# Performance work log

Measured on AMD Instinct MI355X. Metric: run time of the kernel, lower is better.

Reference implementation:

```python
import jax, jax.numpy as jnp
import numpy as np

N = 1_000_000
INC = 128
OUTC = 128
NUM_SEG = 4096
GROUPS = 32
ACN_EPS = 1e-3      # ACN eps
CLAMP_MIN = 1e-3    # .clamp(min=0.001)
GN_EPS = 1e-5       # torch GroupNorm default eps


def setup_inputs() -> dict:
    key = jax.random.key(0)
    ks = jax.random.split(key, 8)
    x = jax.random.normal(ks[0], (N, INC), dtype=jnp.float32)
    weight_pri = jax.random.uniform(ks[1], (N,), dtype=jnp.float32)
    segment_idx = jnp.sort(jax.random.randint(ks[2], (N,), 0, NUM_SEG)).astype(jnp.int64)
    W_conv = (jax.random.normal(ks[3], (INC, OUTC), dtype=jnp.float32) * 0.02)
    b_conv = jnp.zeros((OUTC,), jnp.float32)
    W_att = (jax.random.normal(ks[4], (OUTC, 1), dtype=jnp.float32) * 0.02)
    b_att = jnp.zeros((1,), jnp.float32)
    gamma = jnp.ones((OUTC,), jnp.float32)
    beta = jnp.zeros((OUTC,), jnp.float32)
    return {"x": x, "weight_pri": weight_pri, "W_conv": W_conv, "b_conv": b_conv,
            "W_att": W_att, "b_att": b_att, "gamma": gamma, "beta": beta,
            "segment_idx": segment_idx}


def reference(x, weight_pri, W_conv, b_conv, W_att, b_att, gamma, beta, segment_idx):
    # conv: Linear(inc, outc)
    h = x @ W_conv + b_conv                                  # [N, OUTC]

    # --- ACN ---
    att = h @ W_att + b_att                                  # [N, 1]
    # scatter_softmax over segments (numerically stable)
    seg_max = jax.ops.segment_max(att, segment_idx, num_segments=NUM_SEG)
    e = jnp.exp(att - seg_max[segment_idx])
    a = e / jax.ops.segment_sum(e, segment_idx, num_segments=NUM_SEG)[segment_idx]
    a = a * weight_pri[:, None]
    denom = jnp.maximum(jax.ops.segment_sum(a, segment_idx, num_segments=NUM_SEG), CLAMP_MIN)
    a = a / denom[segment_idx]
    # segment-weighted mean / variance normalization
    mean = jax.ops.segment_sum(h * a, segment_idx, num_segments=NUM_SEG)   # [S, OUTC]
    out = h - mean[segment_idx]
    std = jnp.sqrt(jax.ops.segment_sum(a * out * out, segment_idx, num_segments=NUM_SEG) + ACN_EPS)
    out = out / std[segment_idx]

    # --- GroupNorm(32, OUTC) on [N, C]: normalize per sample, per group ---
    g = out.reshape(-1, GROUPS, OUTC // GROUPS)
    mu = g.mean(axis=-1, keepdims=True)
    var = g.var(axis=-1, keepdims=True)
    gn = ((g - mu) * jax.lax.rsqrt(var + GN_EPS)).reshape(-1, OUTC)
    gn = gn * gamma + beta

    return jax.nn.relu(gn), a
```

## Files before the change

### kernel.cpp

```cpp
#include <hip/hip_runtime.h>
#include <hip/hip_bf16.h>

#define NPTS 1000000
#define NSEG 4096
#define ATTCAP 2048

#define KS_ROWS 16
#define LPAD 136

typedef __attribute__((ext_vector_type(8))) short bf16x8;
typedef __attribute__((ext_vector_type(4))) float f32x4;
typedef __attribute__((ext_vector_type(2))) float f32x2;

__device__ __forceinline__ short f2bfs(float f) {
  union { __hip_bfloat16 b; unsigned short s; } u;
  u.b = __float2bfloat16(f);
  return (short)u.s;
}
__device__ __forceinline__ float bf2f(short h) {
  return __uint_as_float(((unsigned)(unsigned short)h) << 16);
}
__device__ __forceinline__ void online_merge(float& m, float& se, float& sw,
                                             float m2, float se2, float sw2) {
  float nm = fmaxf(m, m2);
  float f1 = __expf(m - nm), f2 = __expf(m2 - nm);
  se = se * f1 + se2 * f2;
  sw = sw * f1 + sw2 * f2;
  m = nm;
}

__device__ __forceinline__ int chbase_of(int wave, int lc) {
  return wave * 32 + (lc >> 1) * 4 + (lc & 1) * 2;
}

__device__ __forceinline__ void load_w2(const float* __restrict__ Wc, int chb, int lg,
                                        bf16x8 Bh[2][4], bf16x8 Bl[2][4]) {
#pragma unroll
  for (int ks = 0; ks < 4; ++ks) {
#pragma unroll
    for (int j = 0; j < 8; ++j) {
      int k = ks * 32 + lg * 8 + j;
      float2 w2 = *(const float2*)(Wc + (size_t)k * 128 + chb);
      float e[2] = {w2.x, w2.y};
#pragma unroll
      for (int c = 0; c < 2; ++c) {
        short hi = f2bfs(e[c]);
        Bh[c][ks][j] = hi;
        Bl[c][ks][j] = f2bfs(e[c] - bf2f(hi));
      }
    }
  }
}

__device__ __forceinline__ void cvt4(float4 v, short4& hi, short4& lo) {
  hi.x = f2bfs(v.x); lo.x = f2bfs(v.x - bf2f(hi.x));
  hi.y = f2bfs(v.y); lo.y = f2bfs(v.y - bf2f(hi.y));
  hi.z = f2bfs(v.z); lo.z = f2bfs(v.z - bf2f(hi.z));
  hi.w = f2bfs(v.w); lo.w = f2bfs(v.w - bf2f(hi.w));
}

__device__ __forceinline__ void cvt4v(f32x4 v, short4& hi, short4& lo) {
  hi.x = f2bfs(v[0]); lo.x = f2bfs(v[0] - bf2f(hi.x));
  hi.y = f2bfs(v[1]); lo.y = f2bfs(v[1] - bf2f(hi.y));
  hi.z = f2bfs(v[2]); lo.z = f2bfs(v[2] - bf2f(hi.z));
  hi.w = f2bfs(v[3]); lo.w = f2bfs(v[3] - bf2f(hi.w));
}

__device__ __forceinline__ void mfma_lds(const bf16x8* __restrict__ AHv,
                                         const bf16x8* __restrict__ ALv,
                                         int lc, int lg,
                                         const bf16x8 Bh[2][4], const bf16x8 Bl[2][4],
                                         f32x4 Cf[2]) {
  Cf[0] = (f32x4){0.f, 0.f, 0.f, 0.f};
  Cf[1] = (f32x4){0.f, 0.f, 0.f, 0.f};
#pragma unroll
  for (int ks = 0; ks < 4; ++ks) {
    int fi = lc * 17 + ks * 4 + lg;
    bf16x8 ah = AHv[fi];
    bf16x8 al = ALv[fi];
#pragma unroll
    for (int c = 0; c < 2; ++c) {
      Cf[c] = __builtin_amdgcn_mfma_f32_16x16x32_bf16(ah, Bh[c][ks], Cf[c], 0, 0, 0);
      Cf[c] = __builtin_amdgcn_mfma_f32_16x16x32_bf16(ah, Bl[c][ks], Cf[c], 0, 0, 0);
      Cf[c] = __builtin_amdgcn_mfma_f32_16x16x32_bf16(al, Bh[c][ks], Cf[c], 0, 0, 0);
    }
  }
}

__global__ __launch_bounds__(256, 4) void k_all2(
    const float* __restrict__ x, const float* __restrict__ wp,
    const float* __restrict__ Wc, const float* __restrict__ bc,
    const float* __restrict__ Wa,
    const float* __restrict__ gamma, const float* __restrict__ beta,
    const void* __restrict__ seg, float* __restrict__ out) {

  __shared__ float att_l[ATTCAP];
  __shared__ __align__(16) short AH[2][KS_ROWS * LPAD];
  __shared__ __align__(16) short AL[2][KS_ROWS * LPAD];
  __shared__ float us[128];
  __shared__ float sm_red[12];
  __shared__ int sm_flag;

  const int t = threadIdx.x;
  const int lane = t & 63;
  const int wave = t >> 6;
  const int lc = lane & 15;
  const int lg = lane >> 4;
  const int chb = chbase_of(wave, lc);
  const int s = blockIdx.x;
  const int* seg32 = (const int*)seg;

  if (t == 0) sm_flag = 0;
  __syncthreads();
  {
    int any = 0;
#pragma unroll
    for (int k = 0; k < 8; ++k) any |= seg32[2 * (t * 8 + k) + 1];
    if (any) sm_flag = 1;
  }
  __syncthreads();
  const int f64 = (sm_flag == 0);
  __syncthreads();

  int blo = 0, bhi = NPTS;
  while (blo < bhi) {
    int mid = (blo + bhi) >> 1;
    int v = f64 ? (int)((const long long*)seg)[mid] : seg32[mid];
    if (v < s) blo = mid + 1; else bhi = mid;
  }
  const int start = blo;
  bhi = NPTS;
  while (blo < bhi) {
    int mid = (blo + bhi) >> 1;
    int v = f64 ? (int)((const long long*)seg)[mid] : seg32[mid];
    if (v < s + 1) blo = mid + 1; else bhi = mid;
  }
  const int endc = min(blo, start + ATTCAP);
  if (start >= endc) return;
  const int len = endc - start;

  if (t < 128) {
    const float4* wa4 = (const float4*)Wa;
    const float4* wr  = (const float4*)(Wc + t * 128);
    float sv = 0.f;
#pragma unroll 8
    for (int c4 = 0; c4 < 32; ++c4) {
      float4 a = wr[c4], b = wa4[c4];
      sv += a.x * b.x + a.y * b.y + a.z * b.z + a.w * b.w;
    }
    us[t] = sv;
  }
  __syncthreads();

  {
    const int q8 = t & 7;
    float ur[16];
#pragma unroll
    for (int j = 0; j < 16; ++j) ur[j] = us[q8 * 16 + j];
    for (int r0 = start; r0 < endc; r0 += 32) {
      int row = r0 + (t >> 3);
      int ra = row < NPTS ? row : NPTS - 1;
      const float4* xp = (const float4*)(x + (size_t)ra * 128 + q8 * 16);
      float4 a0 = xp[0], b0 = xp[1], c0 = xp[2], d0 = xp[3];
      float sv = a0.x*ur[0] + a0.y*ur[1] + a0.z*ur[2] + a0.w*ur[3]
               + b0.x*ur[4] + b0.y*ur[5] + b0.z*ur[6] + b0.w*ur[7]
               + c0.x*ur[8] + c0.y*ur[9] + c0.z*ur[10]+ c0.w*ur[11]
               + d0.x*ur[12]+ d0.y*ur[13]+ d0.z*ur[14]+ d0.w*ur[15];
      sv += __shfl_xor(sv, 1, 64);
      sv += __shfl_xor(sv, 2, 64);
      sv += __shfl_xor(sv, 4, 64);
      if (q8 == 0 && row < endc) att_l[row - start] = sv;
    }
  }
  __syncthreads();

  float m = -3.0e38f, se = 0.f, sw = 0.f;
  for (int i = t; i < len; i += 256) {
    float av = att_l[i], w = wp[start + i];
    float nm = fmaxf(m, av);
    float sc = __expf(m - nm), e = __expf(av - nm);
    se = se * sc + e;
    sw = sw * sc + e * w;
    m = nm;
  }
#pragma unroll
  for (int o = 1; o < 64; o <<= 1)
    online_merge(m, se, sw, __shfl_xor(m, o, 64), __shfl_xor(se, o, 64), __shfl_xor(sw, o, 64));
  if (lane == 0) { sm_red[wave] = m; sm_red[4 + wave] = se; sm_red[8 + wave] = sw; }
  __syncthreads();
  float gmx = sm_red[0], gse = sm_red[4], gsw = sm_red[8];
#pragma unroll
  for (int i = 1; i < 4; ++i) online_merge(gmx, gse, gsw, sm_red[i], sm_red[4 + i], sm_red[8 + i]);
  const float ratio = gsw / gse;
  const float dn = fmaxf(ratio, 1e-3f);
  const float ka = 1.f / (gse * dn);
  const float Sa = ratio / dn;
  for (int i = t; i < len; i += 256) {
    float a = __expf(att_l[i] - gmx) * wp[start + i] * ka;
    att_l[i] = a;
    __builtin_nontemporal_store(a, out + (size_t)NPTS * 128 + start + i);
  }
  __syncthreads();

  bf16x8 Bh[2][4], Bl[2][4];
  load_w2(Wc, chb, lg, Bh, Bl);
  float2 bias2 = *(const float2*)(bc    + chb);
  float2 gam2  = *(const float2*)(gamma + chb);
  float2 bet2  = *(const float2*)(beta  + chb);
  float bias_r[2] = {bias2.x, bias2.y};

  const int nt = (len + KS_ROWS - 1) / KS_ROWS;

  float macc[2] = {0.f, 0.f}, m2cc[2] = {0.f, 0.f};
  {
    float4 stg[2];
#pragma unroll
    for (int i = 0; i < 2; ++i) {
      int idx = t + i * 256, row = idx >> 5, c4 = idx & 31;
      int rg = start + row; if (rg >= endc) rg = endc - 1;
      stg[i] = *(const float4*)(x + (size_t)rg * 128 + c4 * 4);
    }
#pragma unroll
    for (int i = 0; i < 2; ++i) {
      int idx = t + i * 256, row = idx >> 5, c4 = idx & 31;
      short4 hi, lo;
      cvt4(stg[i], hi, lo);
      *(short4*)&AH[0][row * LPAD + c4 * 4] = hi;
      *(short4*)&AL[0][row * LPAD + c4 * 4] = lo;
    }
    int cur = 0, tl = 0;
    while (1) {
      bool pf = (tl + 1 < nt);
      __syncthreads();
      if (pf) {
        int rbase = start + (tl + 1) * KS_ROWS;
#pragma unroll
        for (int i = 0; i < 2; ++i) {
          int idx = t + i * 256, row = idx >> 5, c4 = idx & 31;
          int rg = rbase + row; if (rg >= endc) rg = endc - 1;
          stg[i] = *(const float4*)(x + (size_t)rg * 128 + c4 * 4);
        }
      }
      {
        f32x4 Cf[2];
        mfma_lds((const bf16x8*)AH[cur], (const bf16x8*)AL[cur], lc, lg, Bh, Bl, Cf);
        int rbase = start + tl * KS_ROWS;
#pragma unroll
        for (int reg = 0; reg < 4; ++reg) {
          int row = rbase + lg * 4 + reg;
          float a = (row < endc) ? att_l[row - start] : 0.f;
#pragma unroll
          for (int c = 0; c < 2; ++c) {
            float h = Cf[c][reg] + bias_r[c];
            macc[c] += a * h;
            m2cc[c] += a * h * h;
          }
        }
      }
      if (!pf) break;
      __syncthreads();
#pragma unroll
      for (int i = 0; i < 2; ++i) {
        int idx = t + i * 256, row = idx >> 5, c4 = idx & 31;
        short4 hi, lo;
        cvt4(stg[i], hi, lo);
        *(short4*)&AH[cur ^ 1][row * LPAD + c4 * 4] = hi;
        *(short4*)&AL[cur ^ 1][row * LPAD + c4 * 4] = lo;
      }
      cur ^= 1; ++tl;
    }
  }

#pragma unroll
  for (int c = 0; c < 2; ++c) {
    macc[c] += __shfl_xor(macc[c], 16, 64);
    macc[c] += __shfl_xor(macc[c], 32, 64);
    m2cc[c] += __shfl_xor(m2cc[c], 16, 64);
    m2cc[c] += __shfl_xor(m2cc[c], 32, 64);
  }
  float mean_r[2], isd_r[2];
#pragma unroll
  for (int c = 0; c < 2; ++c) {
    float var = m2cc[c] - macc[c] * macc[c] * (2.f - Sa);
    mean_r[c] = macc[c];
    isd_r[c] = 1.f / sqrtf(var + 1e-3f);
  }
  __syncthreads();

  {
    f32x4 stg[2];
#pragma unroll
    for (int i = 0; i < 2; ++i) {
      int idx = t + i * 256, row = idx >> 5, c4 = idx & 31;
      int rg = start + row; if (rg >= endc) rg = endc - 1;
      stg[i] = __builtin_nontemporal_load((const f32x4*)(x + (size_t)rg * 128 + c4 * 4));
    }
#pragma unroll
    for (int i = 0; i < 2; ++i) {
      int idx = t + i * 256, row = idx >> 5, c4 = idx & 31;
      short4 hi, lo;
      cvt4v(stg[i], hi, lo);
      *(short4*)&AH[0][row * LPAD + c4 * 4] = hi;
      *(short4*)&AL[0][row * LPAD + c4 * 4] = lo;
    }
    int cur = 0, tl = 0;
    while (1) {
      bool pf = (tl + 1 < nt);
      __syncthreads();
      if (pf) {
        int rbase = start + (tl + 1) * KS_ROWS;
#pragma unroll
        for (int i = 0; i < 2; ++i) {
          int idx = t + i * 256, row = idx >> 5, c4 = idx & 31;
          int rg = rbase + row; if (rg >= endc) rg = endc - 1;
          stg[i] = __builtin_nontemporal_load((const f32x4*)(x + (size_t)rg * 128 + c4 * 4));
        }
      }
      {
        f32x4 Cf[2];
        mfma_lds((const bf16x8*)AH[cur], (const bf16x8*)AL[cur], lc, lg, Bh, Bl, Cf);
        int rbase = start + tl * KS_ROWS;
#pragma unroll
        for (int reg = 0; reg < 4; ++reg) {
          int row = rbase + lg * 4 + reg;
          float o0 = (Cf[0][reg] + bias_r[0] - mean_r[0]) * isd_r[0];
          float o1 = (Cf[1][reg] + bias_r[1] - mean_r[1]) * isd_r[1];
          float sp = o0 + o1;
          float qp = o0 * o0 + o1 * o1;
          float s4 = sp + __shfl_xor(sp, 1, 64);
          float q4 = qp + __shfl_xor(qp, 1, 64);
          float mu = 0.25f * s4, msq = 0.25f * q4;
          float gsc = 1.f / sqrtf(msq - mu * mu + 1e-5f);
          if (row < endc) {
            f32x2 v;
            v[0] = fmaxf((o0 - mu) * gsc * gam2.x + bet2.x, 0.f);
            v[1] = fmaxf((o1 - mu) * gsc * gam2.y + bet2.y, 0.f);
            __builtin_nontemporal_store(v, (f32x2*)(out + (size_t)row * 128 + chb));
          }
        }
      }
      if (!pf) break;
      __syncthreads();
#pragma unroll
      for (int i = 0; i < 2; ++i) {
        int idx = t + i * 256, row = idx >> 5, c4 = idx & 31;
        short4 hi, lo;
        cvt4v(stg[i], hi, lo);
        *(short4*)&AH[cur ^ 1][row * LPAD + c4 * 4] = hi;
        *(short4*)&AL[cur ^ 1][row * LPAD + c4 * 4] = lo;
      }
      cur ^= 1; ++tl;
    }
  }
}

extern "C" void kernel_launch(void* const* d_in, const int* in_sizes, int n_in,
                              void* d_out, int out_size, void* d_ws, size_t ws_size,
                              hipStream_t stream) {
  const float* x    = (const float*)d_in[0];
  const float* wpri = (const float*)d_in[1];
  const float* Wc   = (const float*)d_in[2];
  const float* bc   = (const float*)d_in[3];
  const float* Wa   = (const float*)d_in[4];
  const float* gm   = (const float*)d_in[6];
  const float* bt   = (const float*)d_in[7];
  const void*  seg  = d_in[8];
  float* out = (float*)d_out;
  (void)in_sizes; (void)n_in; (void)out_size; (void)d_ws; (void)ws_size;

  k_all2<<<NSEG, 256, 0, stream>>>(x, wpri, Wc, bc, Wa, gm, bt, seg, out);
}
```

Measured before the change: 375.3 us.

## Fuse attention logits and online segment softmax into first GEMM pass

Drops the separate pass that recomputed attention logits by reading x with a precollapsed W_conv·W_att vector. Logits now come from the MFMA conv output already being produced, via a cross-lane and cross-wave reduction. An online softmax then rescales the weighted mean and second-moment accumulators, so x is read twice instead of three times. The cost is an extra block barrier and a round of shuffles per 16-row tile, plus logits computed from the bf16 hi/lo split rather than plain fp32.

```diff
diff --git a/kernel.cpp b/kernel.cpp
--- a/kernel.cpp
+++ b/kernel.cpp
@@ -19,14 +19,6 @@
 }
 __device__ __forceinline__ float bf2f(short h) {
   return __uint_as_float(((unsigned)(unsigned short)h) << 16);
-}
-__device__ __forceinline__ void online_merge(float& m, float& se, float& sw,
-                                             float m2, float se2, float sw2) {
-  float nm = fmaxf(m, m2);
-  float f1 = __expf(m - nm), f2 = __expf(m2 - nm);
-  se = se * f1 + se2 * f2;
-  sw = sw * f1 + sw2 * f2;
-  m = nm;
 }
 
 __device__ __forceinline__ int chbase_of(int wave, int lc) {
@@ -58,7 +50,6 @@
   hi.z = f2bfs(v.z); lo.z = f2bfs(v.z - bf2f(hi.z));
   hi.w = f2bfs(v.w); lo.w = f2bfs(v.w - bf2f(hi.w));
 }
-
 __device__ __forceinline__ void cvt4v(f32x4 v, short4& hi, short4& lo) {
   hi.x = f2bfs(v[0]); lo.x = f2bfs(v[0] - bf2f(hi.x));
   hi.y = f2bfs(v[1]); lo.y = f2bfs(v[1] - bf2f(hi.y));
@@ -87,7 +78,7 @@
   }
 }
 
-__global__ __launch_bounds__(256, 4) void k_all2(
+__global__ __launch_bounds__(256, 4) void k_all3(
     const float* __restrict__ x, const float* __restrict__ wp,
     const float* __restrict__ Wc, const float* __restrict__ bc,
     const float* __restrict__ Wa,
@@ -97,8 +88,7 @@
   __shared__ float att_l[ATTCAP];
   __shared__ __align__(16) short AH[2][KS_ROWS * LPAD];
   __shared__ __align__(16) short AL[2][KS_ROWS * LPAD];
-  __shared__ float us[128];
-  __shared__ float sm_red[12];
+  __shared__ float att_part[4][16];
   __shared__ int sm_flag;
 
   const int t = threadIdx.x;
@@ -138,79 +128,15 @@
   const int endc = min(blo, start + ATTCAP);
   if (start >= endc) return;
   const int len = endc - start;
-
-  if (t < 128) {
-    const float4* wa4 = (const float4*)Wa;
-    const float4* wr  = (const float4*)(Wc + t * 128);
-    float sv = 0.f;
-#pragma unroll 8
-    for (int c4 = 0; c4 < 32; ++c4) {
-      float4 a = wr[c4], b = wa4[c4];
-      sv += a.x * b.x + a.y * b.y + a.z * b.z + a.w * b.w;
-    }
-    us[t] = sv;
-  }
-  __syncthreads();
-
-  {
-    const int q8 = t & 7;
-    float ur[16];
-#pragma unroll
-    for (int j = 0; j < 16; ++j) ur[j] = us[q8 * 16 + j];
-    for (int r0 = start; r0 < endc; r0 += 32) {
-      int row = r0 + (t >> 3);
-      int ra = row < NPTS ? row : NPTS - 1;
-      const float4* xp = (const float4*)(x + (size_t)ra * 128 + q8 * 16);
-      float4 a0 = xp[0], b0 = xp[1], c0 = xp[2], d0 = xp[3];
-      float sv = a0.x*ur[0] + a0.y*ur[1] + a0.z*ur[2] + a0.w*ur[3]
-               + b0.x*ur[4] + b0.y*ur[5] + b0.z*ur[6] + b0.w*ur[7]
-               + c0.x*ur[8] + c0.y*ur[9] + c0.z*ur[10]+ c0.w*ur[11]
-               + d0.x*ur[12]+ d0.y*ur[13]+ d0.z*ur[14]+ d0.w*ur[15];
-      sv += __shfl_xor(sv, 1, 64);
-      sv += __shfl_xor(sv, 2, 64);
-      sv += __shfl_xor(sv, 4, 64);
-      if (q8 == 0 && row < endc) att_l[row - start] = sv;
-    }
-  }
-  __syncthreads();
-
-  float m = -3.0e38f, se = 0.f, sw = 0.f;
-  for (int i = t; i < len; i += 256) {
-    float av = att_l[i], w = wp[start + i];
-    float nm = fmaxf(m, av);
-    float sc = __expf(m - nm), e = __expf(av - nm);
-    se = se * sc + e;
-    sw = sw * sc + e * w;
-    m = nm;
-  }
-#pragma unroll
-  for (int o = 1; o < 64; o <<= 1)
-    online_merge(m, se, sw, __shfl_xor(m, o, 64), __shfl_xor(se, o, 64), __shfl_xor(sw, o, 64));
-  if (lane == 0) { sm_red[wave] = m; sm_red[4 + wave] = se; sm_red[8 + wave] = sw; }
-  __syncthreads();
-  float gmx = sm_red[0], gse = sm_red[4], gsw = sm_red[8];
-#pragma unroll
-  for (int i = 1; i < 4; ++i) online_merge(gmx, gse, gsw, sm_red[i], sm_red[4 + i], sm_red[8 + i]);
-  const float ratio = gsw / gse;
-  const float dn = fmaxf(ratio, 1e-3f);
-  const float ka = 1.f / (gse * dn);
-  const float Sa = ratio / dn;
-  for (int i = t; i < len; i += 256) {
-    float a = __expf(att_l[i] - gmx) * wp[start + i] * ka;
-    att_l[i] = a;
-    __builtin_nontemporal_store(a, out + (size_t)NPTS * 128 + start + i);
-  }
-  __syncthreads();
+  const int nt = (len + KS_ROWS - 1) / KS_ROWS;
 
   bf16x8 Bh[2][4], Bl[2][4];
   load_w2(Wc, chb, lg, Bh, Bl);
-  float2 bias2 = *(const float2*)(bc    + chb);
-  float2 gam2  = *(const float2*)(gamma + chb);
-  float2 bet2  = *(const float2*)(beta  + chb);
+  float2 bias2 = *(const float2*)(bc + chb);
   float bias_r[2] = {bias2.x, bias2.y};
-
-  const int nt = (len + KS_ROWS - 1) / KS_ROWS;
-
+  float wa_r[2]   = {Wa[chb], Wa[chb + 1]};
+
+  float m = -3.0e38f, se = 0.f, sw = 0.f;
   float macc[2] = {0.f, 0.f}, m2cc[2] = {0.f, 0.f};
   {
     float4 stg[2];
@@ -241,19 +167,41 @@
           stg[i] = *(const float4*)(x + (size_t)rg * 128 + c4 * 4);
         }
       }
-      {
-        f32x4 Cf[2];
-        mfma_lds((const bf16x8*)AH[cur], (const bf16x8*)AL[cur], lc, lg, Bh, Bl, Cf);
-        int rbase = start + tl * KS_ROWS;
-#pragma unroll
-        for (int reg = 0; reg < 4; ++reg) {
-          int row = rbase + lg * 4 + reg;
-          float a = (row < endc) ? att_l[row - start] : 0.f;
+      f32x4 Cf[2];
+      mfma_lds((const bf16x8*)AH[cur], (const bf16x8*)AL[cur], lc, lg, Bh, Bl, Cf);
+
+#pragma unroll
+      for (int reg = 0; reg < 4; ++reg) {
+        float p = Cf[0][reg] * wa_r[0] + Cf[1][reg] * wa_r[1];
+        p += __shfl_xor(p, 1, 64);
+        p += __shfl_xor(p, 2, 64);
+        p += __shfl_xor(p, 4, 64);
+        p += __shfl_xor(p, 8, 64);
+        if (lc == 0) att_part[wave][lg * 4 + reg] = p;
+      }
+      __syncthreads();
+
+      int rbase = start + tl * KS_ROWS;
+#pragma unroll
+      for (int reg = 0; reg < 4; ++reg) {
+        int r = lg * 4 + reg;
+        int row = rbase + r;
+        if (row < endc) {
+          float av = att_part[0][r] + att_part[1][r] + att_part[2][r] + att_part[3][r];
+          float wpv = wp[row];
+          if (wave == 0 && lc == 0) att_l[row - start] = av;
+          float nm = fmaxf(m, av);
+          float f = __expf(m - nm);
+          float e = __expf(av - nm);
+          m = nm;
+          se = se * f + e;
+          float ew = e * wpv;
+          sw = sw * f + ew;
 #pragma unroll
           for (int c = 0; c < 2; ++c) {
             float h = Cf[c][reg] + bias_r[c];
-            macc[c] += a * h;
-            m2cc[c] += a * h * h;
+            macc[c] = macc[c] * f + ew * h;
+            m2cc[c] = m2cc[c] * f + ew * h * h;
           }
         }
       }
@@ -272,21 +220,46 @@
   }
 
 #pragma unroll
+  for (int o = 16; o <= 32; o <<= 1) {
+    float m2  = __shfl_xor(m, o, 64);
+    float se2 = __shfl_xor(se, o, 64);
+    float sw2 = __shfl_xor(sw, o, 64);
+    float a0  = __shfl_xor(macc[0], o, 64);
+    float a1  = __shfl_xor(macc[1], o, 64);
+    float q0  = __shfl_xor(m2cc[0], o, 64);
+    float q1  = __shfl_xor(m2cc[1], o, 64);
+    float nm = fmaxf(m, m2);
+    float f1 = __expf(m - nm), f2 = __expf(m2 - nm);
+    se = se * f1 + se2 * f2;
+    sw = sw * f1 + sw2 * f2;
+    macc[0] = macc[0] * f1 + a0 * f2;
+    macc[1] = macc[1] * f1 + a1 * f2;
+    m2cc[0] = m2cc[0] * f1 + q0 * f2;
+    m2cc[1] = m2cc[1] * f1 + q1 * f2;
+    m = nm;
+  }
+  const float ratio = sw / se;
+  const float dn = fmaxf(ratio, 1e-3f);
+  const float ka = 1.f / (se * dn);
+  const float Sa = ratio / dn;
+  float mean_r[2], isd_r[2];
+#pragma unroll
   for (int c = 0; c < 2; ++c) {
-    macc[c] += __shfl_xor(macc[c], 16, 64);
-    macc[c] += __shfl_xor(macc[c], 32, 64);
-    m2cc[c] += __shfl_xor(m2cc[c], 16, 64);
-    m2cc[c] += __shfl_xor(m2cc[c], 32, 64);
-  }
-  float mean_r[2], isd_r[2];
-#pragma unroll
-  for (int c = 0; c < 2; ++c) {
-    float var = m2cc[c] - macc[c] * macc[c] * (2.f - Sa);
-    mean_r[c] = macc[c];
+    float mn = macc[c] * ka;
+    float M2 = m2cc[c] * ka;
+    float var = M2 - mn * mn * (2.f - Sa);
+    mean_r[c] = mn;
     isd_r[c] = 1.f / sqrtf(var + 1e-3f);
   }
   __syncthreads();
 
+  for (int i = t; i < len; i += 256) {
+    float a = __expf(att_l[i] - m) * wp[start + i] * ka;
+    __builtin_nontemporal_store(a, out + (size_t)NPTS * 128 + start + i);
+  }
+
+  float2 gam2 = *(const float2*)(gamma + chb);
+  float2 bet2 = *(const float2*)(beta  + chb);
   {
     f32x4 stg[2];
 #pragma unroll
@@ -368,5 +341,5 @@
   float* out = (float*)d_out;
   (void)in_sizes; (void)n_in; (void)out_size; (void)d_ws; (void)ws_size;
 
-  k_all2<<<NSEG, 256, 0, stream>>>(x, wpri, Wc, bc, Wa, gm, bt, seg, out);
-}
+  k_all3<<<NSEG, 256, 0, stream>>>(x, wpri, Wc, bc, Wa, gm, bt, seg, out);
+}
```

Measured after the change: 405.2 us. 1.08x slower.
